# Kernel tuning notes

Hardware: AMD Instinct MI355X
Metric: run time of the kernel (lower is better)

Reference implementation:

```python
import jax, jax.numpy as jnp
import numpy as np

DIM, HEADS, WS, H, W = 128, 8, 2, 96, 96
HD = DIM // HEADS            # 16
LH = int(HEADS * 0.5)        # 4 low-freq heads
HH = HEADS - LH              # 4 high-freq heads
LD, HDIM = LH * HD, HH * HD  # 64, 64
SCALE = HD ** -0.5


def setup_inputs() -> dict:
    key = jax.random.key(0)
    ks = jax.random.split(key, 8)
    s = 0.02
    return {
        "x": jax.random.normal(ks[0], (1, H * W, DIM), dtype=jnp.float32),
        "restore_w": jax.random.normal(ks[1], (DIM, DIM // (WS * WS)), dtype=jnp.float32) * s,
        "restore_b": jnp.zeros((DIM,), dtype=jnp.float32),
        "l_q_w": jax.random.normal(ks[2], (LD, DIM), dtype=jnp.float32) * s,
        "l_kv_w": jax.random.normal(ks[3], (2 * LD, DIM), dtype=jnp.float32) * s,
        "l_proj_w": jax.random.normal(ks[4], (LD, LD), dtype=jnp.float32) * s,
        "l_proj_b": jnp.zeros((LD,), dtype=jnp.float32),
        "h_qkv_w": jax.random.normal(ks[5], (3 * HDIM, DIM), dtype=jnp.float32) * s,
        "h_proj_w": jax.random.normal(ks[6], (HDIM, HDIM), dtype=jnp.float32) * s,
        "h_proj_b": jnp.zeros((HDIM,), dtype=jnp.float32),
    }


def reference(x, restore_w, restore_b, l_q_w, l_kv_w, l_proj_w, l_proj_b,
              h_qkv_w, h_proj_w, h_proj_b):
    B, N, C = x.shape
    ws, r2 = WS, WS * WS
    xi = x.reshape(B, H, W, C)                       # BHWC (torch uses BCHW; same math)
    Hs, Ws = H // ws, W // ws
    # AvgPool2d(ws, ws)
    low = xi.reshape(B, Hs, ws, Ws, ws, C).mean(axis=(2, 4))  # (B,Hs,Ws,C)
    # PixelShuffle(ws) in BHWC: out[b,hs*r+i,ws*r+j,c] = low[b,hs,ws,c*r2+i*r+j]
    l2h = low.reshape(B, Hs, Ws, C // r2, ws, ws)
    l2h = l2h.transpose(0, 1, 4, 2, 5, 3).reshape(B, H, W, C // r2)
    # 1x1 conv restore, then residual subtract -> high-frequency features
    high = jnp.einsum('bhwi,oi->bhwo', l2h, restore_w) + restore_b - xi  # (B,H,W,C)

    # ---- low-frequency path: full-res queries attend to pooled KV ----
    lq = (x @ l_q_w.T).reshape(B, N, LH, HD).transpose(0, 2, 1, 3)       # (B,LH,N,HD)
    lkv = (low.reshape(B, -1, C) @ l_kv_w.T).reshape(B, -1, 2, LH, HD)
    lkv = lkv.transpose(2, 0, 3, 1, 4)                                   # (2,B,LH,Ns,HD)
    lk, lv = lkv[0], lkv[1]
    lattn = jax.nn.softmax(jnp.einsum('bhnd,bhmd->bhnm', lq, lk) * SCALE, axis=-1)
    lx = jnp.einsum('bhnm,bhmd->bhnd', lattn, lv).transpose(0, 2, 1, 3).reshape(B, H, W, LD)
    lx = lx @ l_proj_w.T + l_proj_b                                      # (B,H,W,LD)

    # ---- high-frequency path: ws x ws windowed attention ----
    hg, wg = H // ws, W // ws
    G = hg * wg
    hw = high.reshape(B, hg, ws, wg, ws, C).transpose(0, 1, 3, 2, 4, 5).reshape(B, G, r2, C)
    qkv = (hw @ h_qkv_w.T).reshape(B, G, r2, 3, HH, HD).transpose(3, 0, 1, 4, 2, 5)
    hq, hk, hv = qkv[0], qkv[1], qkv[2]                                  # (B,G,HH,r2,HD)
    hattn = jax.nn.softmax(jnp.einsum('bghqd,bghkd->bghqk', hq, hk) * SCALE, axis=-1)
    ho = jnp.einsum('bghqk,bghkd->bghqd', hattn, hv).transpose(0, 1, 3, 2, 4)  # (B,G,r2,HH,HD)
    ho = ho.reshape(B, hg, wg, ws, ws, HDIM).transpose(0, 1, 3, 2, 4, 5).reshape(B, H, W, HDIM)
    hx = ho @ h_proj_w.T + h_proj_b                                      # (B,H,W,HDIM)

    return jnp.concatenate([lx, hx], axis=-1).reshape(B, N, C)
```

## Files before the change

kernel.cpp:

```cpp
#include <hip/hip_runtime.h>

#define H_ 96
#define W_ 96
#define NTOK 9216
#define CDIM 128
#define HS_ 48
#define NS_ 2304
#define LHEADS 4
#define HD_ 16
#define LD_ 64
#define SCALE_ 0.25f
#define NPAIR 36864

typedef __attribute__((ext_vector_type(8))) short short8b;
typedef __attribute__((ext_vector_type(4))) float f32x4;
typedef unsigned short ushort_t;

__device__ inline ushort_t f2bf(float x) {
    union { float f; unsigned u; } v; v.f = x;
    unsigned r = v.u + 0x7FFF + ((v.u >> 16) & 1);
    return (ushort_t)(r >> 16);
}

__global__ __launch_bounds__(256)
void k_avgpool(const float* __restrict__ x, float* __restrict__ low) {
    int idx = blockIdx.x * 256 + threadIdx.x;
    if (idx >= NS_ * CDIM) return;
    int c = idx & 127;
    int p = idx >> 7;
    int ws_ = p % HS_, hs = p / HS_;
    int base = ((2 * hs) * W_ + 2 * ws_) * CDIM + c;
    float s = x[base] + x[base + CDIM] + x[base + W_ * CDIM] + x[base + W_ * CDIM + CDIM];
    low[idx] = 0.25f * s;
}

__global__ __launch_bounds__(256)
void k_high(const float* __restrict__ x, const float* __restrict__ low,
            const float* __restrict__ rw, const float* __restrict__ rb,
            float* __restrict__ high) {
    __shared__ float w_s[32 * 128];
    int tid = threadIdx.x;
    #pragma unroll
    for (int k = 0; k < 16; ++k) {
        int idx = tid + k * 256;
        w_s[(idx & 31) * 128 + (idx >> 5)] = rw[idx];
    }
    __syncthreads();
    int base_i = blockIdx.x * 1024;
    #pragma unroll
    for (int k = 0; k < 4; ++k) {
        int idx = base_i + k * 256 + tid;
        int o = idx & 127;
        int n = idx >> 7;
        int h = n / W_, w = n % W_;
        int off = (h & 1) * 2 + (w & 1);
        const float* lrow = low + ((h >> 1) * HS_ + (w >> 1)) * CDIM + off;
        float acc = 0.f;
        #pragma unroll
        for (int ii = 0; ii < 32; ++ii) acc += lrow[ii * 4] * w_s[ii * 128 + o];
        high[idx] = acc + rb[o] - x[idx];
    }
}

__global__ __launch_bounds__(256)
void k_gemm(const float* __restrict__ A, int lda,
            const float* __restrict__ Wt,
            const float* __restrict__ bias,
            float* __restrict__ C, int ldc,
            int K) {
    __shared__ float As[16][68];
    __shared__ float Bs[16][68];
    int tid = threadIdx.x;
    int tx = tid & 15, ty = tid >> 4;
    int m0 = blockIdx.x * 64, n0 = blockIdx.y * 64;
    int lr = tid >> 2;
    int lk = (tid & 3) * 4;
    float acc[4][4] = {};
    for (int kk = 0; kk < K; kk += 16) {
        float4 av = *(const float4*)&A[(m0 + lr) * lda + kk + lk];
        float4 bv = *(const float4*)&Wt[(n0 + lr) * K + kk + lk];
        As[lk + 0][lr] = av.x; As[lk + 1][lr] = av.y;
        As[lk + 2][lr] = av.z; As[lk + 3][lr] = av.w;
        Bs[lk + 0][lr] = bv.x; Bs[lk + 1][lr] = bv.y;
        Bs[lk + 2][lr] = bv.z; Bs[lk + 3][lr] = bv.w;
        __syncthreads();
        #pragma unroll
        for (int k = 0; k < 16; ++k) {
            float a[4], bb[4];
            *(float4*)a  = *(const float4*)&As[k][ty * 4];
            *(float4*)bb = *(const float4*)&Bs[k][tx * 4];
            #pragma unroll
            for (int i = 0; i < 4; ++i)
                #pragma unroll
                for (int j = 0; j < 4; ++j) acc[i][j] += a[i] * bb[j];
        }
        __syncthreads();
    }
    #pragma unroll
    for (int i = 0; i < 4; ++i) {
        int m = m0 + ty * 4 + i;
        #pragma unroll
        for (int j = 0; j < 4; ++j) {
            int n = n0 + tx * 4 + j;
            float v = acc[i][j];
            if (bias) v += bias[n];
            C[m * ldc + n] = v;
        }
    }
}

__global__ __launch_bounds__(256)
void k_gemm_q(const float* __restrict__ A,
              const float* __restrict__ Wt,
              ushort_t* __restrict__ Qb) {
    __shared__ float As[16][68];
    __shared__ float Bs[16][68];
    int tid = threadIdx.x;
    int tx = tid & 15, ty = tid >> 4;
    int m0 = blockIdx.x * 64;
    int lr = tid >> 2;
    int lk = (tid & 3) * 4;
    float acc[4][4] = {};
    for (int kk = 0; kk < CDIM; kk += 16) {
        float4 av = *(const float4*)&A[(m0 + lr) * CDIM + kk + lk];
        float4 bv = *(const float4*)&Wt[lr * CDIM + kk + lk];
        As[lk + 0][lr] = av.x; As[lk + 1][lr] = av.y;
        As[lk + 2][lr] = av.z; As[lk + 3][lr] = av.w;
        Bs[lk + 0][lr] = bv.x; Bs[lk + 1][lr] = bv.y;
        Bs[lk + 2][lr] = bv.z; Bs[lk + 3][lr] = bv.w;
        __syncthreads();
        #pragma unroll
        for (int k = 0; k < 16; ++k) {
            float a[4], bb[4];
            *(float4*)a  = *(const float4*)&As[k][ty * 4];
            *(float4*)bb = *(const float4*)&Bs[k][tx * 4];
            #pragma unroll
            for (int i = 0; i < 4; ++i)
                #pragma unroll
                for (int j = 0; j < 4; ++j) acc[i][j] += a[i] * bb[j];
        }
        __syncthreads();
    }
    #pragma unroll
    for (int i = 0; i < 4; ++i) {
        int m = m0 + ty * 4 + i;
        #pragma unroll
        for (int j = 0; j < 4; ++j) {
            int n = tx * 4 + j;
            int h = n >> 4, d = n & 15;
            Qb[((size_t)h * NTOK + m) * 16 + d] = f2bf(acc[i][j] * SCALE_);
        }
    }
}

__global__ __launch_bounds__(256)
void k_gemm_kv(const float* __restrict__ A,
               const float* __restrict__ Wt,
               ushort_t* __restrict__ Kb, ushort_t* __restrict__ Vt) {
    __shared__ float As[16][68];
    __shared__ float Bs[16][68];
    int tid = threadIdx.x;
    int tx = tid & 15, ty = tid >> 4;
    int m0 = blockIdx.x * 64, n0 = blockIdx.y * 64;
    int lr = tid >> 2;
    int lk = (tid & 3) * 4;
    float acc[4][4] = {};
    for (int kk = 0; kk < CDIM; kk += 16) {
        float4 av = *(const float4*)&A[(m0 + lr) * CDIM + kk + lk];
        float4 bv = *(const float4*)&Wt[(n0 + lr) * CDIM + kk + lk];
        As[lk + 0][lr] = av.x; As[lk + 1][lr] = av.y;
        As[lk + 2][lr] = av.z; As[lk + 3][lr] = av.w;
        Bs[lk + 0][lr] = bv.x; Bs[lk + 1][lr] = bv.y;
        Bs[lk + 2][lr] = bv.z; Bs[lk + 3][lr] = bv.w;
        __syncthreads();
        #pragma unroll
        for (int k = 0; k < 16; ++k) {
            float a[4], bb[4];
            *(float4*)a  = *(const float4*)&As[k][ty * 4];
            *(float4*)bb = *(const float4*)&Bs[k][tx * 4];
            #pragma unroll
            for (int i = 0; i < 4; ++i)
                #pragma unroll
                for (int j = 0; j < 4; ++j) acc[i][j] += a[i] * bb[j];
        }
        __syncthreads();
    }
    #pragma unroll
    for (int i = 0; i < 4; ++i) {
        int m = m0 + ty * 4 + i;
        #pragma unroll
        for (int j = 0; j < 4; ++j) {
            int n = n0 + tx * 4 + j;
            ushort_t v = f2bf(acc[i][j]);
            if (n < 64) {
                int h = n >> 4, d = n & 15;
                Kb[((size_t)h * NS_ + m) * 16 + d] = v;
            } else {
                int h = (n - 64) >> 4, d = (n - 64) & 15;
                Vt[((size_t)h * 16 + d) * NS_ + m] = v;
            }
        }
    }
}

__global__ __launch_bounds__(256)
void k_lattn_mfma(const ushort_t* __restrict__ Qb, const ushort_t* __restrict__ Kb,
                  const ushort_t* __restrict__ Vt, float* __restrict__ lout) {
    __shared__ __align__(16) ushort_t P_lds[4][16][32];
    int tid = threadIdx.x;
    int wid = tid >> 6;
    int lane = tid & 63;
    int g = lane >> 4, c = lane & 15;
    int head = blockIdx.x / (NTOK / 64);
    int qb = blockIdx.x % (NTOK / 64);
    int q0 = qb * 64 + wid * 16;

    short8b zf = {0, 0, 0, 0, 0, 0, 0, 0};
    f32x4 zc = {0.f, 0.f, 0.f, 0.f};

    short8b qfrag = zf;
    if (g < 2)
        qfrag = *(const short8b*)(Qb + ((size_t)head * NTOK + q0 + c) * 16 + g * 8);

    const ushort_t* kbase = Kb + (size_t)head * NS_ * 16;
    const ushort_t* vbase = Vt + ((size_t)head * 16 + c) * NS_;

    f32x4 o = zc;
    float lsum[4] = {0.f, 0.f, 0.f, 0.f};

#define LOADT(KA, KB, VV, kt) do {                                            \
    if (g < 2) {                                                              \
        KA = *(const short8b*)(kbase + ((kt) + c) * 16 + g * 8);              \
        KB = *(const short8b*)(kbase + ((kt) + 16 + c) * 16 + g * 8);         \
    } else { KA = zf; KB = zf; }                                              \
    VV = *(const short8b*)(vbase + (kt) + 8 * g);                             \
} while (0)

#define COMPT(KA, KB, VV) do {                                                \
    f32x4 s0 = __builtin_amdgcn_mfma_f32_16x16x32_bf16(qfrag, KA, zc, 0, 0, 0); \
    f32x4 s1 = __builtin_amdgcn_mfma_f32_16x16x32_bf16(qfrag, KB, zc, 0, 0, 0); \
    _Pragma("unroll")                                                         \
    for (int r = 0; r < 4; ++r) {                                             \
        float p0 = __expf(s0[r]);                                             \
        float p1 = __expf(s1[r]);                                             \
        lsum[r] += p0 + p1;                                                   \
        P_lds[wid][4 * g + r][c] = f2bf(p0);                                  \
        P_lds[wid][4 * g + r][16 + c] = f2bf(p1);                             \
    }                                                                         \
    short8b pa = *(const short8b*)&P_lds[wid][c][8 * g];                      \
    o = __builtin_amdgcn_mfma_f32_16x16x32_bf16(pa, VV, o, 0, 0, 0);          \
} while (0)

    short8b kA, kB, vA, kA2, kB2, vA2;
    LOADT(kA, kB, vA, 0);
    int kt = 0;
    for (kt = 0; kt + 64 < NS_; kt += 64) {
        LOADT(kA2, kB2, vA2, kt + 32);
        COMPT(kA, kB, vA);
        LOADT(kA, kB, vA, kt + 64);
        COMPT(kA2, kB2, vA2);
    }
    LOADT(kA2, kB2, vA2, kt + 32);
    COMPT(kA, kB, vA);
    COMPT(kA2, kB2, vA2);
#undef LOADT
#undef COMPT

    #pragma unroll
    for (int r = 0; r < 4; ++r) {
        float s = lsum[r];
        s += __shfl_xor(s, 1);
        s += __shfl_xor(s, 2);
        s += __shfl_xor(s, 4);
        s += __shfl_xor(s, 8);
        lout[(size_t)(q0 + 4 * g + r) * LD_ + head * HD_ + c] = o[r] / s;
    }
}

__global__ __launch_bounds__(256)
void k_hattn(const float* __restrict__ qkv, float* __restrict__ ho) {
    int idx = blockIdx.x * 256 + threadIdx.x;
    if (idx >= NPAIR) return;
    int t = idx & 3;
    int hh = (idx >> 2) & 3;
    int g = idx >> 4;
    int gh = g / 48, gw = g % 48;
    int nq = (2 * gh + (t >> 1)) * W_ + 2 * gw + (t & 1);
    float q[HD_];
    #pragma unroll
    for (int d = 0; d < HD_; ++d) q[d] = qkv[nq * 192 + hh * HD_ + d];
    float e[4], esum = 0.f;
    int nk[4];
    #pragma unroll
    for (int kt = 0; kt < 4; ++kt) {
        nk[kt] = (2 * gh + (kt >> 1)) * W_ + 2 * gw + (kt & 1);
        float s = 0.f;
        #pragma unroll
        for (int d = 0; d < HD_; ++d) s += q[d] * qkv[nk[kt] * 192 + 64 + hh * HD_ + d];
        e[kt] = __expf(s * SCALE_);
        esum += e[kt];
    }
    float inv = 1.f / esum;
    float o[HD_] = {};
    #pragma unroll
    for (int kt = 0; kt < 4; ++kt) {
        float pkt = e[kt] * inv;
        #pragma unroll
        for (int d = 0; d < HD_; ++d) o[d] += pkt * qkv[nk[kt] * 192 + 128 + hh * HD_ + d];
    }
    #pragma unroll
    for (int d = 0; d < HD_; ++d) ho[nq * 64 + hh * HD_ + d] = o[d];
}

extern "C" void kernel_launch(void* const* d_in, const int* in_sizes, int n_in,
                              void* d_out, int out_size, void* d_ws, size_t ws_size,
                              hipStream_t stream) {
    const float* x        = (const float*)d_in[0];
    const float* restore_w = (const float*)d_in[1];
    const float* restore_b = (const float*)d_in[2];
    const float* l_q_w    = (const float*)d_in[3];
    const float* l_kv_w   = (const float*)d_in[4];
    const float* l_proj_w = (const float*)d_in[5];
    const float* l_proj_b = (const float*)d_in[6];
    const float* h_qkv_w  = (const float*)d_in[7];
    const float* h_proj_w = (const float*)d_in[8];
    const float* h_proj_b = (const float*)d_in[9];
    float* out = (float*)d_out;

    float* ws    = (float*)d_ws;
    float* low   = ws;
    float* high  = ws + 294912;
    float* hqkv  = ws + 1474560;
    float* ho    = ws + 3244032;
    float* lout  = ws + 3833856;
    ushort_t* Qb = (ushort_t*)(ws + 4423680);
    ushort_t* Kb = (ushort_t*)(ws + 4718592);
    ushort_t* Vt = (ushort_t*)(ws + 4792320);

    k_avgpool<<<(NS_ * CDIM + 255) / 256, 256, 0, stream>>>(x, low);
    k_high<<<NTOK * CDIM / 1024, 256, 0, stream>>>(x, low, restore_w, restore_b, high);
    k_gemm_kv<<<dim3(NS_ / 64, 2), 256, 0, stream>>>(low, l_kv_w, Kb, Vt);

    k_gemm<<<dim3(NTOK / 64, 3), 256, 0, stream>>>(high, CDIM, h_qkv_w, nullptr, hqkv, 192, CDIM);
    k_hattn<<<(NPAIR + 255) / 256, 256, 0, stream>>>(hqkv, ho);
    k_gemm<<<dim3(NTOK / 64, 1), 256, 0, stream>>>(ho, LD_, h_proj_w, h_proj_b, out + 64, CDIM, LD_);

    k_gemm_q<<<NTOK / 64, 256, 0, stream>>>(x, l_q_w, Qb);
    k_lattn_mfma<<<LHEADS * (NTOK / 64), 256, 0, stream>>>(Qb, Kb, Vt, lout);
    k_gemm<<<dim3(NTOK / 64, 1), 256, 0, stream>>>(lout, LD_, l_proj_w, l_proj_b, out, CDIM, LD_);
}
```

Measured before the change: 182.1 us.

## Split low-freq attention KV across two blocks and pack P stores

Splits the low-frequency attention over the pooled key dimension into two halves run as separate blocks (grid y=2). Each block writes unnormalized partial outputs and row sums, and a new combine kernel adds the halves and normalizes. It also permutes V's layout so each lane stores P as one packed 32-bit pair, halving the LDS stores, with a padded LDS row. This aims to raise parallelism and shorten each block's serial loop, at the cost of an extra launch and extra global traffic for the partials.

```diff
diff --git a/kernel.cpp b/kernel.cpp
--- a/kernel.cpp
+++ b/kernel.cpp
@@ -6,6 +6,7 @@
 #define CDIM 128
 #define HS_ 48
 #define NS_ 2304
+#define KSP 1152
 #define LHEADS 4
 #define HD_ 16
 #define LD_ 64
@@ -197,7 +198,9 @@
                 Kb[((size_t)h * NS_ + m) * 16 + d] = v;
             } else {
                 int h = (n - 64) >> 4, d = (n - 64) & 15;
-                Vt[((size_t)h * 16 + d) * NS_ + m] = v;
+                int blk = m >> 5, km = m & 31;
+                int pos = ((km & 15) << 1) | (km >> 4);
+                Vt[((size_t)h * 16 + d) * NS_ + blk * 32 + pos] = v;
             }
         }
     }
@@ -205,14 +208,16 @@
 
 __global__ __launch_bounds__(256)
 void k_lattn_mfma(const ushort_t* __restrict__ Qb, const ushort_t* __restrict__ Kb,
-                  const ushort_t* __restrict__ Vt, float* __restrict__ lout) {
-    __shared__ __align__(16) ushort_t P_lds[4][16][32];
+                  const ushort_t* __restrict__ Vt, float* __restrict__ pacc,
+                  float* __restrict__ psum) {
+    __shared__ __align__(16) unsigned P_lds[4][16][20];
     int tid = threadIdx.x;
     int wid = tid >> 6;
     int lane = tid & 63;
     int g = lane >> 4, c = lane & 15;
     int head = blockIdx.x / (NTOK / 64);
     int qb = blockIdx.x % (NTOK / 64);
+    int split = blockIdx.y;
     int q0 = qb * 64 + wid * 16;
 
     short8b zf = {0, 0, 0, 0, 0, 0, 0, 0};
@@ -222,8 +227,9 @@
     if (g < 2)
         qfrag = *(const short8b*)(Qb + ((size_t)head * NTOK + q0 + c) * 16 + g * 8);
 
-    const ushort_t* kbase = Kb + (size_t)head * NS_ * 16;
-    const ushort_t* vbase = Vt + ((size_t)head * 16 + c) * NS_;
+    const int kb0 = split * KSP;
+    const ushort_t* kbase = Kb + (size_t)head * NS_ * 16 + (size_t)kb0 * 16;
+    const ushort_t* vbase = Vt + ((size_t)head * 16 + c) * NS_ + kb0;
 
     f32x4 o = zc;
     float lsum[4] = {0.f, 0.f, 0.f, 0.f};
@@ -244,17 +250,16 @@
         float p0 = __expf(s0[r]);                                             \
         float p1 = __expf(s1[r]);                                             \
         lsum[r] += p0 + p1;                                                   \
-        P_lds[wid][4 * g + r][c] = f2bf(p0);                                  \
-        P_lds[wid][4 * g + r][16 + c] = f2bf(p1);                             \
+        P_lds[wid][4 * g + r][c] = ((unsigned)f2bf(p1) << 16) | f2bf(p0);     \
     }                                                                         \
-    short8b pa = *(const short8b*)&P_lds[wid][c][8 * g];                      \
+    short8b pa = *(const short8b*)&P_lds[wid][c][4 * g];                      \
     o = __builtin_amdgcn_mfma_f32_16x16x32_bf16(pa, VV, o, 0, 0, 0);          \
 } while (0)
 
     short8b kA, kB, vA, kA2, kB2, vA2;
     LOADT(kA, kB, vA, 0);
     int kt = 0;
-    for (kt = 0; kt + 64 < NS_; kt += 64) {
+    for (kt = 0; kt + 64 < KSP; kt += 64) {
         LOADT(kA2, kB2, vA2, kt + 32);
         COMPT(kA, kB, vA);
         LOADT(kA, kB, vA, kt + 64);
@@ -273,8 +278,25 @@
         s += __shfl_xor(s, 2);
         s += __shfl_xor(s, 4);
         s += __shfl_xor(s, 8);
-        lout[(size_t)(q0 + 4 * g + r) * LD_ + head * HD_ + c] = o[r] / s;
-    }
+        size_t p = ((size_t)split * LHEADS + head) * NTOK + q0 + 4 * g + r;
+        pacc[p * 16 + c] = o[r];
+        if (c == 0) psum[p] = s;
+    }
+}
+
+__global__ __launch_bounds__(256)
+void k_lattn_combine(const float* __restrict__ pacc, const float* __restrict__ psum,
+                     float* __restrict__ lout) {
+    int idx = blockIdx.x * 256 + threadIdx.x;
+    if (idx >= LHEADS * NTOK * HD_) return;
+    int d = idx & 15;
+    int q = (idx >> 4) % NTOK;
+    int h = (idx >> 4) / NTOK;
+    size_t p0 = ((size_t)0 * LHEADS + h) * NTOK + q;
+    size_t p1 = ((size_t)1 * LHEADS + h) * NTOK + q;
+    float a = pacc[p0 * 16 + d] + pacc[p1 * 16 + d];
+    float s = psum[p0] + psum[p1];
+    lout[(size_t)q * LD_ + h * HD_ + d] = a / s;
 }
 
 __global__ __launch_bounds__(256)
@@ -336,6 +358,8 @@
     ushort_t* Qb = (ushort_t*)(ws + 4423680);
     ushort_t* Kb = (ushort_t*)(ws + 4718592);
     ushort_t* Vt = (ushort_t*)(ws + 4792320);
+    float* pacc  = ws + 4866048;
+    float* psum  = ws + 6045696;
 
     k_avgpool<<<(NS_ * CDIM + 255) / 256, 256, 0, stream>>>(x, low);
     k_high<<<NTOK * CDIM / 1024, 256, 0, stream>>>(x, low, restore_w, restore_b, high);
@@ -346,6 +370,7 @@
     k_gemm<<<dim3(NTOK / 64, 1), 256, 0, stream>>>(ho, LD_, h_proj_w, h_proj_b, out + 64, CDIM, LD_);
 
     k_gemm_q<<<NTOK / 64, 256, 0, stream>>>(x, l_q_w, Qb);
-    k_lattn_mfma<<<LHEADS * (NTOK / 64), 256, 0, stream>>>(Qb, Kb, Vt, lout);
+    k_lattn_mfma<<<dim3(LHEADS * (NTOK / 64), 2), 256, 0, stream>>>(Qb, Kb, Vt, pacc, psum);
+    k_lattn_combine<<<(LHEADS * NTOK * HD_ + 255) / 256, 256, 0, stream>>>(pacc, psum, lout);
     k_gemm<<<dim3(NTOK / 64, 1), 256, 0, stream>>>(lout, LD_, l_proj_w, l_proj_b, out, CDIM, LD_);
 }
```

Measured after the change: 178.9 us. No clear change (-1.7%).
